# Optimization experiments

Measured on AMD Instinct MI355X. Metric: run time of the kernel, lower is better.

The kernel has to match this reference:

```python
import jax, jax.numpy as jnp
import numpy as np

WS = 16          # window_size
HS = 8           # halo_size
NH = 4           # num_heads
DIM = 128
WSH = WS + 2 * HS  # 32, window with halo
B, H, W = 2, 128, 128


def _rel_pos_index():
    # static relative-position index table, (WSH^2, WSH^2), int
    r = np.arange(-HS, WS + HS)
    coords = np.stack(np.meshgrid(r, r, indexing='ij'))        # (2, WSH, WSH)
    cf = coords.reshape(2, -1)                                  # (2, WSH^2)
    rel = (cf[:, :, None] - cf[:, None, :]).transpose(1, 2, 0)  # (L, L, 2)
    rel = rel.copy()
    rel[..., 0] += WS + HS - 1
    rel[..., 1] += WS + HS - 1
    rel[..., 0] *= 2 * WS + 2 * HS - 1
    return rel.sum(-1)  # (1024, 1024)

_RPI = _rel_pos_index()


def setup_inputs() -> dict:
    key = jax.random.key(0)
    ks = jax.random.split(key, 10)
    p = lambda k, shp: (jax.random.normal(k, shp, dtype=jnp.float32) * 0.02)
    return {
        'x': jax.random.normal(ks[0], (B, H, W, DIM), dtype=jnp.float32),
        'Wq': p(ks[1], (DIM, DIM)), 'bq': jnp.zeros((DIM,), jnp.float32),
        'Wk': p(ks[2], (DIM, DIM)), 'bk': jnp.zeros((DIM,), jnp.float32),
        'Wv': p(ks[3], (DIM, DIM)), 'bv': jnp.zeros((DIM,), jnp.float32),
        'Wp': p(ks[4], (DIM, DIM)), 'bp': jnp.zeros((DIM,), jnp.float32),
        'bias_table': p(ks[5], ((2 * WS + 2 * HS - 1) ** 2, NH)),
        'shift_size': 0,
    }


def reference(x, Wq, bq, Wk, bk, Wv, bv, Wp, bp, bias_table, shift_size):
    Bx, Hx, Wx, C = x.shape
    hd = C // NH
    scale = hd ** -0.5
    if shift_size > 0:
        x = jnp.roll(x, (-shift_size, -shift_size), axis=(1, 2))
    # reflect-pad by halo and gather overlapping 32x32 windows (stride 16)
    xp = jnp.pad(x, ((0, 0), (HS, HS), (HS, HS), (0, 0)), mode='reflect')
    nWh, nWw = Hx // WS, Wx // WS
    rows = (jnp.arange(nWh) * WS)[:, None] + jnp.arange(WSH)   # (nWh, 32)
    cols = (jnp.arange(nWw) * WS)[:, None] + jnp.arange(WSH)   # (nWw, 32)
    w = xp[:, rows]                 # (B, nWh, 32, Wp, C)
    w = w[:, :, :, cols]            # (B, nWh, 32, nWw, 32, C)
    w = w.transpose(0, 1, 3, 2, 4, 5).reshape(-1, WSH, WSH, C)  # (B*nW, 32, 32, C)
    center = w[:, HS:HS + WS, HS:HS + WS].reshape(-1, WS * WS, C)   # (nWb, 256, C)
    kv = w.reshape(-1, WSH * WSH, C)                                # (nWb, 1024, C)
    q = (center @ Wq.T + bq).reshape(-1, WS * WS, NH, hd).transpose(0, 2, 1, 3)
    k = (kv @ Wk.T + bk).reshape(-1, WSH * WSH, NH, hd).transpose(0, 2, 1, 3)
    v = (kv @ Wv.T + bv).reshape(-1, WSH * WSH, NH, hd).transpose(0, 2, 1, 3)
    attn = jnp.einsum('bhqd,bhkd->bhqk', q, k) * scale   # (nWb, H, 256, 1024)
    bias = bias_table[_RPI.reshape(-1)].reshape(WSH * WSH, WSH * WSH, NH)
    bias = bias.transpose(2, 0, 1)                        # (H, 1024, 1024)
    start = HS * 2 * WS                                   # 256, as in source
    attn = attn + bias[:, start:start + WS * WS, :][None]
    attn = jax.nn.softmax(attn, axis=-1)
    out = jnp.einsum('bhqk,bhkd->bhqd', attn, v)
    out = out.transpose(0, 2, 1, 3).reshape(-1, WS * WS, C)
    out = out @ Wp.T + bp
    out = out.reshape(Bx, nWh, nWw, WS, WS, C).transpose(0, 1, 3, 2, 4, 5)
    out = out.reshape(Bx, Hx, Wx, C)
    if shift_size > 0:
        out = jnp.roll(out, (shift_size, shift_size), axis=(1, 2))
    return out
```

## Files before the change

### kernel.cpp

```cpp
#include <hip/hip_runtime.h>


typedef unsigned short ushort_t;
typedef __attribute__((ext_vector_type(8))) short bf16x8;
typedef __attribute__((ext_vector_type(4))) float floatx4;

#define NHEADS 4
#define BTBL 2209
#define PK 64
#define LOG2E 1.4426950408889634f
#define QSCALE (0.17677669529663687f * LOG2E)

__device__ __forceinline__ int reflect_idx(int p) {
    p = (p < 0) ? -p : p;
    p = (p > 127) ? 254 - p : p;
    return p;
}

__device__ __forceinline__ ushort_t f2b(float x) {
    unsigned u = __float_as_uint(x);
    return (ushort_t)((u + 0x7fffu + ((u >> 16) & 1u)) >> 16);
}

__global__ __launch_bounds__(256) void prep(
    const float* __restrict__ Wq, const float* __restrict__ Wk,
    const float* __restrict__ Wv, const float* __restrict__ Wp,
    const float* __restrict__ bq, const float* __restrict__ bk,
    const float* __restrict__ bv, const float* __restrict__ bp,
    const float* __restrict__ bt,
    ushort_t* __restrict__ Wqkv, ushort_t* __restrict__ Wpb,
    float* __restrict__ bqkv, float* __restrict__ bpb,
    ushort_t* __restrict__ bf)
{
    if (blockIdx.x < 257) {
        int idx = blockIdx.x * 256 + threadIdx.x;
        if (idx < 16384)       Wqkv[idx] = f2b(Wq[idx]);
        else if (idx < 32768)  Wqkv[idx] = f2b(Wk[idx - 16384]);
        else if (idx < 49152)  Wqkv[idx] = f2b(Wv[idx - 32768]);
        else if (idx < 65536)  Wpb[idx - 49152] = f2b(Wp[idx - 49152]);
        else {
            int e = idx - 65536;
            for (int k = e; k < 512; k += 256) {
                if (k < 128)      bqkv[k] = bq[k];
                else if (k < 256) bqkv[k] = bk[k - 128];
                else if (k < 384) bqkv[k] = bv[k - 256];
                else              bpb[k - 384] = bp[k - 384];
            }
        }
    } else {
        int idx  = (blockIdx.x - 257) * 256 + threadIdx.x;
        int lane = idx & 63;
        int qtw  = (idx >> 6) & 15;
        int kt   = (idx >> 10) & 63;
        int h    = (idx >> 16) & 3;
        int q     = qtw * 16 + (lane & 15);
        int kbase = kt * 16 + ((lane >> 4) << 2);
        unsigned v[4];
        #pragma unroll
        for (int r = 0; r < 4; ++r) {
            int key = kbase + r;
            int kr = key >> 5, kc = key & 31;
            int bidx = ((q >> 5) + 31 - kr) * 47 + (q & 31) - kc + 23;
            if (bidx < 0) bidx += BTBL;
            v[r] = f2b(bt[bidx * NHEADS + h] * LOG2E);
        }
        uint2 o;
        o.x = v[0] | (v[1] << 16);
        o.y = v[2] | (v[3] << 16);
        *(uint2*)&bf[(size_t)idx * 4] = o;
    }
}

__global__ __launch_bounds__(256) void gemm_qkv(
    const float* __restrict__ X, const ushort_t* __restrict__ W,
    const float* __restrict__ bias,
    ushort_t* __restrict__ Qb, ushort_t* __restrict__ Kb,
    ushort_t* __restrict__ Vb)
{
    __shared__ ushort_t Xs[128 * 136];

    const int t    = threadIdx.x;
    const int w    = t >> 6;
    const int lane = t & 63;
    const int quad = lane >> 4;
    const int l15  = lane & 15;
    const int m0   = blockIdx.x * 128;

    #pragma unroll
    for (int i = 0; i < 16; ++i) {
        int s = t + i * 256;
        int row = s >> 5, c4 = s & 31;
        float4 v = *(const float4*)&X[(size_t)(m0 + row) * 128 + c4 * 4];
        uint2 pk;
        pk.x = (unsigned)f2b(v.x) | ((unsigned)f2b(v.y) << 16);
        pk.y = (unsigned)f2b(v.z) | ((unsigned)f2b(v.w) << 16);
        *(uint2*)&Xs[row * 136 + c4 * 4] = pk;
    }
    __syncthreads();

    #pragma unroll 1
    for (int nb = 0; nb < 3; ++nb) {
        const float sc = (nb == 0) ? QSCALE : 1.0f;

        floatx4 acc[2][8];
        #pragma unroll
        for (int nt = 0; nt < 8; ++nt) {
            floatx4 bv = *(const floatx4*)&bias[nb * 128 + nt * 16 + quad * 4];
            acc[0][nt] = bv;
            acc[1][nt] = bv;
        }

        #pragma unroll
        for (int kc = 0; kc < 4; ++kc) {
            bf16x8 af[2], bfr[8];
            #pragma unroll
            for (int mt = 0; mt < 2; ++mt)
                af[mt] = *(const bf16x8*)&Xs[(w * 32 + mt * 16 + l15) * 136 + kc * 32 + quad * 8];
            #pragma unroll
            for (int nt = 0; nt < 8; ++nt)
                bfr[nt] = *(const bf16x8*)&W[(size_t)(nb * 128 + nt * 16 + l15) * 128 + kc * 32 + quad * 8];
            #pragma unroll
            for (int mt = 0; mt < 2; ++mt)
                #pragma unroll
                for (int nt = 0; nt < 8; ++nt)
                    acc[mt][nt] = __builtin_amdgcn_mfma_f32_16x16x32_bf16(bfr[nt], af[mt], acc[mt][nt], 0, 0, 0);
        }

        #pragma unroll
        for (int mt = 0; mt < 2; ++mt) {
            int m = m0 + w * 32 + mt * 16 + l15;
            #pragma unroll
            for (int nt = 0; nt < 8; ++nt) {
                int n = nt * 16 + quad * 4;
                uint2 pk;
                pk.x = (unsigned)f2b(acc[mt][nt][0] * sc) |
                       ((unsigned)f2b(acc[mt][nt][1] * sc) << 16);
                pk.y = (unsigned)f2b(acc[mt][nt][2] * sc) |
                       ((unsigned)f2b(acc[mt][nt][3] * sc) << 16);
                if (nb == 0) {
                    *(uint2*)&Qb[(size_t)m * 128 + n] = pk;
                } else {
                    size_t off = (((size_t)(n >> 5) << 15) + m) * 32 + (n & 31);
                    if (nb == 1) *(uint2*)&Kb[off] = pk;
                    else         *(uint2*)&Vb[off] = pk;
                }
            }
        }
    }
}

__global__ __launch_bounds__(256) void gemm_proj(
    const ushort_t* __restrict__ X, const ushort_t* __restrict__ W,
    const float* __restrict__ bias, float* __restrict__ out)
{
    __shared__ ushort_t Xs[128 * 136];

    const int t    = threadIdx.x;
    const int w    = t >> 6;
    const int lane = t & 63;
    const int quad = lane >> 4;
    const int l15  = lane & 15;
    const int m0   = blockIdx.x * 128;

    #pragma unroll
    for (int i = 0; i < 8; ++i) {
        int s = t + i * 256;
        int row = s >> 4, c8 = s & 15;
        *(int4*)&Xs[row * 136 + c8 * 8] =
            *(const int4*)&X[(size_t)(m0 + row) * 128 + c8 * 8];
    }
    __syncthreads();

    floatx4 acc[2][8];
    #pragma unroll
    for (int nt = 0; nt < 8; ++nt) {
        floatx4 bv = *(const floatx4*)&bias[nt * 16 + quad * 4];
        acc[0][nt] = bv;
        acc[1][nt] = bv;
    }

    #pragma unroll
    for (int kc = 0; kc < 4; ++kc) {
        bf16x8 af[2], bfr[8];
        #pragma unroll
        for (int mt = 0; mt < 2; ++mt)
            af[mt] = *(const bf16x8*)&Xs[(w * 32 + mt * 16 + l15) * 136 + kc * 32 + quad * 8];
        #pragma unroll
        for (int nt = 0; nt < 8; ++nt)
            bfr[nt] = *(const bf16x8*)&W[(size_t)(nt * 16 + l15) * 128 + kc * 32 + quad * 8];
        #pragma unroll
        for (int mt = 0; mt < 2; ++mt)
            #pragma unroll
            for (int nt = 0; nt < 8; ++nt)
                acc[mt][nt] = __builtin_amdgcn_mfma_f32_16x16x32_bf16(bfr[nt], af[mt], acc[mt][nt], 0, 0, 0);
    }

    #pragma unroll
    for (int mt = 0; mt < 2; ++mt) {
        int m = m0 + w * 32 + mt * 16 + l15;
        #pragma unroll
        for (int nt = 0; nt < 8; ++nt) {
            int n = nt * 16 + quad * 4;
            float4 v;
            v.x = acc[mt][nt][0]; v.y = acc[mt][nt][1];
            v.z = acc[mt][nt][2]; v.w = acc[mt][nt][3];
            *(float4*)&out[(size_t)m * 128 + n] = v;
        }
    }
}

__global__ __launch_bounds__(256, 2) void halo_attn(
    const ushort_t* __restrict__ Qb,
    const ushort_t* __restrict__ Kb,
    const ushort_t* __restrict__ Vb,
    const ushort_t* __restrict__ biasf,
    ushort_t* __restrict__ O)
{
    __shared__ ushort_t P_lds[4 * 64 * PK];
    __shared__ ushort_t Vt_lds[4 * 32 * PK];

    const int t    = threadIdx.x;
    const int wave = t >> 6;
    const int lane = t & 63;
    const int quad = lane >> 4;
    const int l15  = lane & 15;
    const int swz  = (l15 & 7) << 3;

    const int win  = blockIdx.x;
    const int head = blockIdx.y;
    const int b    = win >> 6;
    const int wh   = (win >> 3) & 7;
    const int ww   = win & 7;
    const size_t hbase = (size_t)head << 15;

    bf16x8 qf[4];
    int qpix[4];
    #pragma unroll
    for (int qt = 0; qt < 4; ++qt) {
        int q_abs = wave * 64 + qt * 16 + l15;
        int gy = wh * 16 + (q_abs >> 4), gx = ww * 16 + (q_abs & 15);
        int pix = (b * 128 + gy) * 128 + gx;
        qpix[qt] = pix;
        qf[qt] = *(const bf16x8*)(Qb + (size_t)pix * 128 + head * 32 + quad * 8);
    }

    floatx4 Oa[2][4];
    #pragma unroll
    for (int dt = 0; dt < 2; ++dt)
        #pragma unroll
        for (int qt = 0; qt < 4; ++qt)
            Oa[dt][qt] = (floatx4)0.f;
    float l[4] = {0.f, 0.f, 0.f, 0.f};

    ushort_t* Pw  = P_lds  + wave * 64 * PK;
    ushort_t* Vtw = Vt_lds + wave * 32 * PK;

    for (int c = 0; c < 16; ++c) {
        {
            int keyv = c * 64 + lane;
            int ky = reflect_idx(wh * 16 + (keyv >> 5) - 8);
            int kx = reflect_idx(ww * 16 + (keyv & 31) - 8);
            int pixv = (b * 128 + ky) * 128 + kx;
            const int4* vp4 = (const int4*)(Vb + ((hbase + pixv) << 5));
            int4 vw0 = vp4[0], vw1 = vp4[1], vw2 = vp4[2], vw3 = vp4[3];
            const ushort_t* vs0 = (const ushort_t*)&vw0;
            const ushort_t* vs1 = (const ushort_t*)&vw1;
            const ushort_t* vs2 = (const ushort_t*)&vw2;
            const ushort_t* vs3 = (const ushort_t*)&vw3;
            #pragma unroll
            for (int d = 0; d < 8; ++d) {
                int cs = lane ^ (d << 3);
                Vtw[(d +  0) * PK + cs] = vs0[d];
                Vtw[(d +  8) * PK + cs] = vs1[d];
                Vtw[(d + 16) * PK + cs] = vs2[d];
                Vtw[(d + 24) * PK + cs] = vs3[d];
            }
        }

        bf16x8 kf[4];
        #pragma unroll
        for (int kt = 0; kt < 4; ++kt) {
            int key = c * 64 + kt * 16 + l15;
            int ky = reflect_idx(wh * 16 + (key >> 5) - 8);
            int kx = reflect_idx(ww * 16 + (key & 31) - 8);
            int pixk = (b * 128 + ky) * 128 + kx;
            kf[kt] = *(const bf16x8*)(Kb + ((hbase + pixk) << 5) + quad * 8);
        }

        floatx4 S[4][4];
        #pragma unroll
        for (int kt = 0; kt < 4; ++kt) {
            int kt_abs = c * 4 + kt;
            #pragma unroll
            for (int qt = 0; qt < 4; ++qt) {
                size_t off = ((((size_t)head * 64 + kt_abs) * 16 + (wave * 4 + qt)) * 64 + lane) * 4;
                uint2 bb = *(const uint2*)(biasf + off);
                floatx4 s;
                s[0] = __uint_as_float(bb.x << 16);
                s[1] = __uint_as_float(bb.x & 0xffff0000u);
                s[2] = __uint_as_float(bb.y << 16);
                s[3] = __uint_as_float(bb.y & 0xffff0000u);
                S[kt][qt] = s;
            }
        }
        #pragma unroll
        for (int kt = 0; kt < 4; ++kt)
            #pragma unroll
            for (int qt = 0; qt < 4; ++qt)
                S[kt][qt] = __builtin_amdgcn_mfma_f32_16x16x32_bf16(kf[kt], qf[qt], S[kt][qt], 0, 0, 0);

        #pragma unroll
        for (int qt = 0; qt < 4; ++qt) {
            float ls = 0.f;
            #pragma unroll
            for (int kt = 0; kt < 4; ++kt) {
                #pragma unroll
                for (int r = 0; r < 4; ++r) {
                    float p = __builtin_amdgcn_exp2f(S[kt][qt][r]);
                    S[kt][qt][r] = p;
                    ls += p;
                }
            }
            l[qt] += ls;
            #pragma unroll
            for (int kt = 0; kt < 4; ++kt) {
                uint2 pk;
                pk.x = __builtin_amdgcn_perm(__float_as_uint(S[kt][qt][1]),
                                             __float_as_uint(S[kt][qt][0]), 0x07060302u);
                pk.y = __builtin_amdgcn_perm(__float_as_uint(S[kt][qt][3]),
                                             __float_as_uint(S[kt][qt][2]), 0x07060302u);
                *(uint2*)&Pw[(qt * 16 + l15) * PK + ((kt * 16 + quad * 4) ^ swz)] = pk;
            }
        }

        #pragma unroll
        for (int ks = 0; ks < 2; ++ks) {
            bf16x8 vf[2];
            #pragma unroll
            for (int dt = 0; dt < 2; ++dt)
                vf[dt] = *(const bf16x8*)&Vtw[(dt * 16 + l15) * PK + ((ks * 32 + quad * 8) ^ swz)];
            #pragma unroll
            for (int qt = 0; qt < 4; ++qt) {
                bf16x8 pf = *(const bf16x8*)&Pw[(qt * 16 + l15) * PK + ((ks * 32 + quad * 8) ^ swz)];
                #pragma unroll
                for (int dt = 0; dt < 2; ++dt)
                    Oa[dt][qt] = __builtin_amdgcn_mfma_f32_16x16x32_bf16(vf[dt], pf, Oa[dt][qt], 0, 0, 0);
            }
        }
    }

    #pragma unroll
    for (int qt = 0; qt < 4; ++qt) {
        float lq = l[qt];
        lq += __shfl_xor(lq, 16);
        lq += __shfl_xor(lq, 32);
        float inv = 1.0f / lq;
        #pragma unroll
        for (int dt = 0; dt < 2; ++dt) {
            uint2 pk;
            pk.x = (unsigned)f2b(Oa[dt][qt][0] * inv) | ((unsigned)f2b(Oa[dt][qt][1] * inv) << 16);
            pk.y = (unsigned)f2b(Oa[dt][qt][2] * inv) | ((unsigned)f2b(Oa[dt][qt][3] * inv) << 16);
            *(uint2*)(O + (size_t)qpix[qt] * 128 + head * 32 + dt * 16 + quad * 4) = pk;
        }
    }
}

extern "C" void kernel_launch(void* const* d_in, const int* in_sizes, int n_in,
                              void* d_out, int out_size, void* d_ws, size_t ws_size,
                              hipStream_t stream)
{
    const float* x          = (const float*)d_in[0];
    const float* Wq         = (const float*)d_in[1];
    const float* bq         = (const float*)d_in[2];
    const float* Wk         = (const float*)d_in[3];
    const float* bk         = (const float*)d_in[4];
    const float* Wv         = (const float*)d_in[5];
    const float* bv         = (const float*)d_in[6];
    const float* Wp         = (const float*)d_in[7];
    const float* bp         = (const float*)d_in[8];
    const float* bias_table = (const float*)d_in[9];
    float* out = (float*)d_out;

    char* ws = (char*)d_ws;
    ushort_t* Wqkv = (ushort_t*)(ws);
    ushort_t* Wpb  = (ushort_t*)(ws + 98304);
    float*    bqkv = (float*)   (ws + 131072);
    float*    bpb  = (float*)   (ws + 132608);
    ushort_t* Qb   = (ushort_t*)(ws + 133120);
    ushort_t* Kb   = (ushort_t*)(ws + 8521728);
    ushort_t* Vb   = (ushort_t*)(ws + 16910336);
    ushort_t* Ob   = (ushort_t*)(ws + 25298944);
    ushort_t* bf   = (ushort_t*)(ws + 33687552);

    prep<<<dim3(1281), dim3(256), 0, stream>>>(Wq, Wk, Wv, Wp, bq, bk, bv, bp,
                                               bias_table, Wqkv, Wpb, bqkv, bpb, bf);
    gemm_qkv<<<dim3(256), dim3(256), 0, stream>>>(x, Wqkv, bqkv, Qb, Kb, Vb);
    halo_attn<<<dim3(128, NHEADS), dim3(256), 0, stream>>>(Qb, Kb, Vb, bf, Ob);
    gemm_proj<<<dim3(256), dim3(256), 0, stream>>>(Ob, Wpb, bpb, out);
}
```

Baseline: 158.1 us.

## Split query rows across two blocks and share the V transpose across waves

The halo attention grid gains a z dimension of two, so each block handles 128 query pixels and each wave handles 32 instead of 64. The per-wave V transpose is replaced by a block-cooperative one: each thread loads one 16-byte chunk of V and writes it into a double-buffered shared tile, followed by a __syncthreads. This cuts register and LDS use so occupancy can rise to four blocks per CU. In exchange, every block redundantly reloads K and V for its window, and a block-wide barrier is added per key chunk.

```diff
diff --git a/kernel.cpp b/kernel.cpp
--- a/kernel.cpp
+++ b/kernel.cpp
@@ -209,15 +209,15 @@
     }
 }
 
-__global__ __launch_bounds__(256, 2) void halo_attn(
+__global__ __launch_bounds__(256, 4) void halo_attn(
     const ushort_t* __restrict__ Qb,
     const ushort_t* __restrict__ Kb,
     const ushort_t* __restrict__ Vb,
     const ushort_t* __restrict__ biasf,
     ushort_t* __restrict__ O)
 {
-    __shared__ ushort_t P_lds[4 * 64 * PK];
-    __shared__ ushort_t Vt_lds[4 * 32 * PK];
+    __shared__ ushort_t P_lds[4 * 32 * PK];
+    __shared__ ushort_t Vt_lds[2 * 32 * PK];
 
     const int t    = threadIdx.x;
     const int wave = t >> 6;
@@ -228,54 +228,44 @@
 
     const int win  = blockIdx.x;
     const int head = blockIdx.y;
+    const int qh   = blockIdx.z;
     const int b    = win >> 6;
     const int wh   = (win >> 3) & 7;
     const int ww   = win & 7;
     const size_t hbase = (size_t)head << 15;
 
-    bf16x8 qf[4];
-    int qpix[4];
-    #pragma unroll
-    for (int qt = 0; qt < 4; ++qt) {
-        int q_abs = wave * 64 + qt * 16 + l15;
+    const int vkey = t & 63;
+    const int vchk = t >> 6;
+    const int vrow = vkey >> 5;
+    const int vkx  = reflect_idx(ww * 16 + (vkey & 31) - 8);
+
+    bf16x8 qf[2];
+    int qpix[2];
+    #pragma unroll
+    for (int qt = 0; qt < 2; ++qt) {
+        int q_abs = qh * 128 + wave * 32 + qt * 16 + l15;
         int gy = wh * 16 + (q_abs >> 4), gx = ww * 16 + (q_abs & 15);
         int pix = (b * 128 + gy) * 128 + gx;
         qpix[qt] = pix;
         qf[qt] = *(const bf16x8*)(Qb + (size_t)pix * 128 + head * 32 + quad * 8);
     }
 
-    floatx4 Oa[2][4];
+    floatx4 Oa[2][2];
     #pragma unroll
     for (int dt = 0; dt < 2; ++dt)
         #pragma unroll
-        for (int qt = 0; qt < 4; ++qt)
+        for (int qt = 0; qt < 2; ++qt)
             Oa[dt][qt] = (floatx4)0.f;
-    float l[4] = {0.f, 0.f, 0.f, 0.f};
-
-    ushort_t* Pw  = P_lds  + wave * 64 * PK;
-    ushort_t* Vtw = Vt_lds + wave * 32 * PK;
+    float l[2] = {0.f, 0.f};
+
+    ushort_t* Pw = P_lds + wave * 32 * PK;
 
     for (int c = 0; c < 16; ++c) {
-        {
-            int keyv = c * 64 + lane;
-            int ky = reflect_idx(wh * 16 + (keyv >> 5) - 8);
-            int kx = reflect_idx(ww * 16 + (keyv & 31) - 8);
-            int pixv = (b * 128 + ky) * 128 + kx;
-            const int4* vp4 = (const int4*)(Vb + ((hbase + pixv) << 5));
-            int4 vw0 = vp4[0], vw1 = vp4[1], vw2 = vp4[2], vw3 = vp4[3];
-            const ushort_t* vs0 = (const ushort_t*)&vw0;
-            const ushort_t* vs1 = (const ushort_t*)&vw1;
-            const ushort_t* vs2 = (const ushort_t*)&vw2;
-            const ushort_t* vs3 = (const ushort_t*)&vw3;
-            #pragma unroll
-            for (int d = 0; d < 8; ++d) {
-                int cs = lane ^ (d << 3);
-                Vtw[(d +  0) * PK + cs] = vs0[d];
-                Vtw[(d +  8) * PK + cs] = vs1[d];
-                Vtw[(d + 16) * PK + cs] = vs2[d];
-                Vtw[(d + 24) * PK + cs] = vs3[d];
-            }
-        }
+        const int par = c & 1;
+
+        int kyv = reflect_idx(wh * 16 + 2 * c + vrow - 8);
+        int pixv = (b * 128 + kyv) * 128 + vkx;
+        int4 vw = *(const int4*)(Vb + ((hbase + pixv) << 5) + vchk * 8);
 
         bf16x8 kf[4];
         #pragma unroll
@@ -287,13 +277,14 @@
             kf[kt] = *(const bf16x8*)(Kb + ((hbase + pixk) << 5) + quad * 8);
         }
 
-        floatx4 S[4][4];
+        floatx4 S[4][2];
         #pragma unroll
         for (int kt = 0; kt < 4; ++kt) {
             int kt_abs = c * 4 + kt;
             #pragma unroll
-            for (int qt = 0; qt < 4; ++qt) {
-                size_t off = ((((size_t)head * 64 + kt_abs) * 16 + (wave * 4 + qt)) * 64 + lane) * 4;
+            for (int qt = 0; qt < 2; ++qt) {
+                int qrow = qh * 8 + wave * 2 + qt;
+                size_t off = ((((size_t)head * 64 + kt_abs) * 16 + qrow) * 64 + lane) * 4;
                 uint2 bb = *(const uint2*)(biasf + off);
                 floatx4 s;
                 s[0] = __uint_as_float(bb.x << 16);
@@ -306,11 +297,11 @@
         #pragma unroll
         for (int kt = 0; kt < 4; ++kt)
             #pragma unroll
-            for (int qt = 0; qt < 4; ++qt)
+            for (int qt = 0; qt < 2; ++qt)
                 S[kt][qt] = __builtin_amdgcn_mfma_f32_16x16x32_bf16(kf[kt], qf[qt], S[kt][qt], 0, 0, 0);
 
         #pragma unroll
-        for (int qt = 0; qt < 4; ++qt) {
+        for (int qt = 0; qt < 2; ++qt) {
             float ls = 0.f;
             #pragma unroll
             for (int kt = 0; kt < 4; ++kt) {
@@ -333,24 +324,38 @@
             }
         }
 
-        #pragma unroll
-        for (int ks = 0; ks < 2; ++ks) {
-            bf16x8 vf[2];
-            #pragma unroll
-            for (int dt = 0; dt < 2; ++dt)
-                vf[dt] = *(const bf16x8*)&Vtw[(dt * 16 + l15) * PK + ((ks * 32 + quad * 8) ^ swz)];
-            #pragma unroll
-            for (int qt = 0; qt < 4; ++qt) {
-                bf16x8 pf = *(const bf16x8*)&Pw[(qt * 16 + l15) * PK + ((ks * 32 + quad * 8) ^ swz)];
+        {
+            ushort_t* Vp = Vt_lds + par * 32 * PK;
+            const ushort_t* vs = (const ushort_t*)&vw;
+            #pragma unroll
+            for (int j = 0; j < 8; ++j) {
+                int d = vchk * 8 + j;
+                Vp[d * PK + (vkey ^ (j << 3))] = vs[j];
+            }
+        }
+        __syncthreads();
+
+        {
+            const ushort_t* Vp = Vt_lds + par * 32 * PK;
+            #pragma unroll
+            for (int ks = 0; ks < 2; ++ks) {
+                bf16x8 vf[2];
                 #pragma unroll
                 for (int dt = 0; dt < 2; ++dt)
-                    Oa[dt][qt] = __builtin_amdgcn_mfma_f32_16x16x32_bf16(vf[dt], pf, Oa[dt][qt], 0, 0, 0);
-            }
-        }
-    }
-
-    #pragma unroll
-    for (int qt = 0; qt < 4; ++qt) {
+                    vf[dt] = *(const bf16x8*)&Vp[(dt * 16 + l15) * PK + ((ks * 32 + quad * 8) ^ swz)];
+                #pragma unroll
+                for (int qt = 0; qt < 2; ++qt) {
+                    bf16x8 pf = *(const bf16x8*)&Pw[(qt * 16 + l15) * PK + ((ks * 32 + quad * 8) ^ swz)];
+                    #pragma unroll
+                    for (int dt = 0; dt < 2; ++dt)
+                        Oa[dt][qt] = __builtin_amdgcn_mfma_f32_16x16x32_bf16(vf[dt], pf, Oa[dt][qt], 0, 0, 0);
+                }
+            }
+        }
+    }
+
+    #pragma unroll
+    for (int qt = 0; qt < 2; ++qt) {
         float lq = l[qt];
         lq += __shfl_xor(lq, 16);
         lq += __shfl_xor(lq, 32);
@@ -395,6 +400,6 @@
     prep<<<dim3(1281), dim3(256), 0, stream>>>(Wq, Wk, Wv, Wp, bq, bk, bv, bp,
                                                bias_table, Wqkv, Wpb, bqkv, bpb, bf);
     gemm_qkv<<<dim3(256), dim3(256), 0, stream>>>(x, Wqkv, bqkv, Qb, Kb, Vb);
-    halo_attn<<<dim3(128, NHEADS), dim3(256), 0, stream>>>(Qb, Kb, Vb, bf, Ob);
+    halo_attn<<<dim3(128, NHEADS, 2), dim3(256), 0, stream>>>(Qb, Kb, Vb, bf, Ob);
     gemm_proj<<<dim3(256), dim3(256), 0, stream>>>(Ob, Wpb, bpb, out);
 }
```

Measured after the change: 161.1 us. No clear change (+1.9%).

## Prefetch next K/V chunk into registers with double-buffered loop

Applied to the files above, without the earlier changes.

Restructures the attention key loop so K fragments and V rows for chunk c+1 are loaded into a second register set while chunk c is computed, ping-ponging between two buffers. It also hoists the reflect-index column computations out of the loop. The aim is to hide global-memory load latency behind the MFMA and softmax work. The cost is higher register pressure, which may lower occupancy or cause spills, plus one redundant wrap-around load of chunk 0 on the last iteration.

```diff
diff --git a/kernel.cpp b/kernel.cpp
--- a/kernel.cpp
+++ b/kernel.cpp
@@ -233,6 +233,11 @@
     const int ww   = win & 7;
     const size_t hbase = (size_t)head << 15;
 
+    const int kxA = reflect_idx(ww * 16 + l15 - 8);
+    const int kxB = reflect_idx(ww * 16 + l15 + 8);
+    const int vkx = reflect_idx(ww * 16 + (lane & 31) - 8);
+    const int vrow = lane >> 5;
+
     bf16x8 qf[4];
     int qpix[4];
     #pragma unroll
@@ -255,18 +260,28 @@
     ushort_t* Pw  = P_lds  + wave * 64 * PK;
     ushort_t* Vtw = Vt_lds + wave * 32 * PK;
 
-    for (int c = 0; c < 16; ++c) {
+    struct KVreg { bf16x8 k[4]; int4 v[4]; };
+
+    auto load = [&](int c, KVreg& r) {
+        int ky0 = reflect_idx(wh * 16 + 2 * c - 8);
+        int ky1 = reflect_idx(wh * 16 + 2 * c - 7);
+        r.k[0] = *(const bf16x8*)(Kb + ((hbase + (b * 128 + ky0) * 128 + kxA) << 5) + quad * 8);
+        r.k[1] = *(const bf16x8*)(Kb + ((hbase + (b * 128 + ky0) * 128 + kxB) << 5) + quad * 8);
+        r.k[2] = *(const bf16x8*)(Kb + ((hbase + (b * 128 + ky1) * 128 + kxA) << 5) + quad * 8);
+        r.k[3] = *(const bf16x8*)(Kb + ((hbase + (b * 128 + ky1) * 128 + kxB) << 5) + quad * 8);
+        int kyv = reflect_idx(wh * 16 + 2 * c + vrow - 8);
+        const int4* vp = (const int4*)(Vb + ((hbase + (b * 128 + kyv) * 128 + vkx) << 5));
+        r.v[0] = vp[0]; r.v[1] = vp[1]; r.v[2] = vp[2]; r.v[3] = vp[3];
+    };
+
+    auto body = [&](int c, KVreg& cur, KVreg& nxt, int cn) {
+        load(cn, nxt);
+
         {
-            int keyv = c * 64 + lane;
-            int ky = reflect_idx(wh * 16 + (keyv >> 5) - 8);
-            int kx = reflect_idx(ww * 16 + (keyv & 31) - 8);
-            int pixv = (b * 128 + ky) * 128 + kx;
-            const int4* vp4 = (const int4*)(Vb + ((hbase + pixv) << 5));
-            int4 vw0 = vp4[0], vw1 = vp4[1], vw2 = vp4[2], vw3 = vp4[3];
-            const ushort_t* vs0 = (const ushort_t*)&vw0;
-            const ushort_t* vs1 = (const ushort_t*)&vw1;
-            const ushort_t* vs2 = (const ushort_t*)&vw2;
-            const ushort_t* vs3 = (const ushort_t*)&vw3;
+            const ushort_t* vs0 = (const ushort_t*)&cur.v[0];
+            const ushort_t* vs1 = (const ushort_t*)&cur.v[1];
+            const ushort_t* vs2 = (const ushort_t*)&cur.v[2];
+            const ushort_t* vs3 = (const ushort_t*)&cur.v[3];
             #pragma unroll
             for (int d = 0; d < 8; ++d) {
                 int cs = lane ^ (d << 3);
@@ -275,16 +290,6 @@
                 Vtw[(d + 16) * PK + cs] = vs2[d];
                 Vtw[(d + 24) * PK + cs] = vs3[d];
             }
-        }
-
-        bf16x8 kf[4];
-        #pragma unroll
-        for (int kt = 0; kt < 4; ++kt) {
-            int key = c * 64 + kt * 16 + l15;
-            int ky = reflect_idx(wh * 16 + (key >> 5) - 8);
-            int kx = reflect_idx(ww * 16 + (key & 31) - 8);
-            int pixk = (b * 128 + ky) * 128 + kx;
-            kf[kt] = *(const bf16x8*)(Kb + ((hbase + pixk) << 5) + quad * 8);
         }
 
         floatx4 S[4][4];
@@ -307,7 +312,7 @@
         for (int kt = 0; kt < 4; ++kt)
             #pragma unroll
             for (int qt = 0; qt < 4; ++qt)
-                S[kt][qt] = __builtin_amdgcn_mfma_f32_16x16x32_bf16(kf[kt], qf[qt], S[kt][qt], 0, 0, 0);
+                S[kt][qt] = __builtin_amdgcn_mfma_f32_16x16x32_bf16(cur.k[kt], qf[qt], S[kt][qt], 0, 0, 0);
 
         #pragma unroll
         for (int qt = 0; qt < 4; ++qt) {
@@ -347,6 +352,14 @@
                     Oa[dt][qt] = __builtin_amdgcn_mfma_f32_16x16x32_bf16(vf[dt], pf, Oa[dt][qt], 0, 0, 0);
             }
         }
+    };
+
+    KVreg A, B;
+    load(0, A);
+    #pragma unroll 1
+    for (int c = 0; c < 16; c += 2) {
+        body(c,     A, B, c + 1);
+        body(c + 1, B, A, (c + 2) & 15);
     }
 
     #pragma unroll
```

Measured after the change: 168.2 us. +6.4%, slower.

## Feed softmax probabilities to PV MFMA from registers, drop P LDS round-trip

Applied to the files above, without the earlier changes.

The exponentiated scores are packed to bf16 and used directly as the B operand of 16x16x16 bf16 MFMAs, since the S accumulator layout already matches the K=16 operand layout. This removes the per-wave P shared-memory buffer and its writes and reads. The precomputed bias layout is also reordered so each lane loads all four q-tiles' bias with two 16-byte loads instead of four 8-byte loads. The cost is twice as many PV MFMA instructions, each with half the K depth, plus narrower V loads from LDS.

```diff
diff --git a/kernel.cpp b/kernel.cpp
--- a/kernel.cpp
+++ b/kernel.cpp
@@ -3,6 +3,7 @@
 
 typedef unsigned short ushort_t;
 typedef __attribute__((ext_vector_type(8))) short bf16x8;
+typedef __attribute__((ext_vector_type(4))) short bf16x4;
 typedef __attribute__((ext_vector_type(4))) float floatx4;
 
 #define NHEADS 4
@@ -49,11 +50,13 @@
         }
     } else {
         int idx  = (blockIdx.x - 257) * 256 + threadIdx.x;
-        int lane = idx & 63;
-        int qtw  = (idx >> 6) & 15;
+        int qt   = idx & 3;
+        int lane = (idx >> 2) & 63;
+        int wave = (idx >> 8) & 3;
         int kt   = (idx >> 10) & 63;
         int h    = (idx >> 16) & 3;
-        int q     = qtw * 16 + (lane & 15);
+        int qrow  = wave * 4 + qt;
+        int q     = qrow * 16 + (lane & 15);
         int kbase = kt * 16 + ((lane >> 4) << 2);
         unsigned v[4];
         #pragma unroll
@@ -216,7 +219,6 @@
     const ushort_t* __restrict__ biasf,
     ushort_t* __restrict__ O)
 {
-    __shared__ ushort_t P_lds[4 * 64 * PK];
     __shared__ ushort_t Vt_lds[4 * 32 * PK];
 
     const int t    = threadIdx.x;
@@ -252,7 +254,6 @@
             Oa[dt][qt] = (floatx4)0.f;
     float l[4] = {0.f, 0.f, 0.f, 0.f};
 
-    ushort_t* Pw  = P_lds  + wave * 64 * PK;
     ushort_t* Vtw = Vt_lds + wave * 32 * PK;
 
     for (int c = 0; c < 16; ++c) {
@@ -291,15 +292,21 @@
         #pragma unroll
         for (int kt = 0; kt < 4; ++kt) {
             int kt_abs = c * 4 + kt;
+            size_t boff = ((((size_t)head * 64 + kt_abs) * 4 + wave) * 64 + lane) * 16;
+            int4 blo = *(const int4*)&biasf[boff];
+            int4 bhi = *(const int4*)&biasf[boff + 8];
+            unsigned bx[4], by[4];
+            bx[0] = (unsigned)blo.x; by[0] = (unsigned)blo.y;
+            bx[1] = (unsigned)blo.z; by[1] = (unsigned)blo.w;
+            bx[2] = (unsigned)bhi.x; by[2] = (unsigned)bhi.y;
+            bx[3] = (unsigned)bhi.z; by[3] = (unsigned)bhi.w;
             #pragma unroll
             for (int qt = 0; qt < 4; ++qt) {
-                size_t off = ((((size_t)head * 64 + kt_abs) * 16 + (wave * 4 + qt)) * 64 + lane) * 4;
-                uint2 bb = *(const uint2*)(biasf + off);
                 floatx4 s;
-                s[0] = __uint_as_float(bb.x << 16);
-                s[1] = __uint_as_float(bb.x & 0xffff0000u);
-                s[2] = __uint_as_float(bb.y << 16);
-                s[3] = __uint_as_float(bb.y & 0xffff0000u);
+                s[0] = __uint_as_float(bx[qt] << 16);
+                s[1] = __uint_as_float(bx[qt] & 0xffff0000u);
+                s[2] = __uint_as_float(by[qt] << 16);
+                s[3] = __uint_as_float(by[qt] & 0xffff0000u);
                 S[kt][qt] = s;
             }
         }
@@ -310,41 +317,28 @@
                 S[kt][qt] = __builtin_amdgcn_mfma_f32_16x16x32_bf16(kf[kt], qf[qt], S[kt][qt], 0, 0, 0);
 
         #pragma unroll
-        for (int qt = 0; qt < 4; ++qt) {
-            float ls = 0.f;
-            #pragma unroll
-            for (int kt = 0; kt < 4; ++kt) {
-                #pragma unroll
-                for (int r = 0; r < 4; ++r) {
-                    float p = __builtin_amdgcn_exp2f(S[kt][qt][r]);
-                    S[kt][qt][r] = p;
-                    ls += p;
-                }
-            }
-            l[qt] += ls;
-            #pragma unroll
-            for (int kt = 0; kt < 4; ++kt) {
+        for (int kt = 0; kt < 4; ++kt) {
+            bf16x4 vf[2];
+            #pragma unroll
+            for (int dt = 0; dt < 2; ++dt)
+                vf[dt] = *(const bf16x4*)&Vtw[(dt * 16 + l15) * PK + ((kt * 16 + quad * 4) ^ swz)];
+            #pragma unroll
+            for (int qt = 0; qt < 4; ++qt) {
+                float p0 = __builtin_amdgcn_exp2f(S[kt][qt][0]);
+                float p1 = __builtin_amdgcn_exp2f(S[kt][qt][1]);
+                float p2 = __builtin_amdgcn_exp2f(S[kt][qt][2]);
+                float p3 = __builtin_amdgcn_exp2f(S[kt][qt][3]);
+                l[qt] += (p0 + p1) + (p2 + p3);
                 uint2 pk;
-                pk.x = __builtin_amdgcn_perm(__float_as_uint(S[kt][qt][1]),
-                                             __float_as_uint(S[kt][qt][0]), 0x07060302u);
-                pk.y = __builtin_amdgcn_perm(__float_as_uint(S[kt][qt][3]),
-                                             __float_as_uint(S[kt][qt][2]), 0x07060302u);
-                *(uint2*)&Pw[(qt * 16 + l15) * PK + ((kt * 16 + quad * 4) ^ swz)] = pk;
-            }
-        }
-
-        #pragma unroll
-        for (int ks = 0; ks < 2; ++ks) {
-            bf16x8 vf[2];
-            #pragma unroll
-            for (int dt = 0; dt < 2; ++dt)
-                vf[dt] = *(const bf16x8*)&Vtw[(dt * 16 + l15) * PK + ((ks * 32 + quad * 8) ^ swz)];
-            #pragma unroll
-            for (int qt = 0; qt < 4; ++qt) {
-                bf16x8 pf = *(const bf16x8*)&Pw[(qt * 16 + l15) * PK + ((ks * 32 + quad * 8) ^ swz)];
+                pk.x = __builtin_amdgcn_perm(__float_as_uint(p1),
+                                             __float_as_uint(p0), 0x07060302u);
+                pk.y = __builtin_amdgcn_perm(__float_as_uint(p3),
+                                             __float_as_uint(p2), 0x07060302u);
+                bf16x4 pf = *(bf16x4*)&pk;
                 #pragma unroll
                 for (int dt = 0; dt < 2; ++dt)
-                    Oa[dt][qt] = __builtin_amdgcn_mfma_f32_16x16x32_bf16(vf[dt], pf, Oa[dt][qt], 0, 0, 0);
+                    Oa[dt][qt] = __builtin_amdgcn_mfma_f32_16x16x16bf16_1k(
+                        vf[dt], pf, Oa[dt][qt], 0, 0, 0);
             }
         }
     }
```

Measured after the change: 173.3 us. 1.1x slower.
